# Optimization experiments

Measured on AMD Instinct MI355X. Metric: run time of the kernel, lower is better.

Reference implementation:

```python
import jax, jax.numpy as jnp
import numpy as np

HIDDEN, INPUT_DIM, OUTPUT_DIM, SEQ_LEN, BATCH = 1024, 1, 10, 784, 512


def make_discrete_hippo(N, L):
    # HiPPO-LegS matrix: A[n,k] = -sqrt(2n+1)sqrt(2k+1) for n>k, -(n+1) on diag; B[n]=sqrt(2n+1)
    q = np.arange(N, dtype=np.float64)
    P = np.sqrt(1.0 + 2.0 * q)
    A = -(np.tril(np.outer(P, P)) - np.diag(q))
    B = P[:, None]  # (N, 1)
    # bilinear (Tustin) discretization with step = 1/L
    step = 1.0 / L
    I = np.eye(N)
    M = np.linalg.inv(I - (step / 2.0) * A)
    Ad = M @ (I + (step / 2.0) * A)
    Bd = step * (M @ B)
    return jnp.asarray(Ad, jnp.float32), jnp.asarray(Bd, jnp.float32)


def setup_inputs() -> dict:
    key = jax.random.key(0)
    k1, k2, k3 = jax.random.split(key, 3)
    x = jax.random.normal(k1, (BATCH, SEQ_LEN, 1), jnp.float32)
    # C: xavier_uniform-like scale, shape (input_dim, hidden_dim)
    C = jax.random.normal(k2, (INPUT_DIM, HIDDEN), jnp.float32) / np.sqrt(HIDDEN).astype(np.float32)
    # final Dense(output_dim): kernel (input_dim, output_dim), bias (output_dim,)
    W = jax.random.normal(k3, (INPUT_DIM, OUTPUT_DIM), jnp.float32)
    b = jnp.zeros((OUTPUT_DIM,), jnp.float32)
    return {"x": x, "C": C, "W": W, "b": b}


def reference(x, C, W, b):
    Ad, Bd = make_discrete_hippo(HIDDEN, SEQ_LEN)  # constants (not learned)
    AdT = Ad.T                       # (N, N)
    Bvec = Bd[:, 0]                  # (N,)
    us = jnp.moveaxis(x[..., 0], 1, 0)  # (seq, batch) -- scan over time axis
    h0 = jnp.zeros((x.shape[0], HIDDEN), x.dtype)

    def step(h, u):
        # h_next = tanh(A h^T + B u)^T  ==  tanh(h @ A^T + u[:,None]*B)
        h_next = jnp.tanh(h @ AdT + u[:, None] * Bvec[None, :])  # (batch, N)
        y = h_next @ C.T                                         # (batch, input_dim)
        return h_next, y

    _, ys = jax.lax.scan(step, h0, us)  # ys: (seq, batch, input_dim)
    # Dense applied to all timesteps then [:, -1, :] == Dense on last timestep
    return ys[-1] @ W + b  # (batch, output_dim)
```

## Files before the change

### kernel.cpp

```cpp
#include <hip/hip_runtime.h>
#include <math.h>


#define SEQ     784
#define OUT_DIM 10
#define NW      4
#define CH      16
#define NCH     (SEQ/CH)
#define EPL     4

#if __has_builtin(__builtin_amdgcn_exp2f)
#define EXP2F(x) __builtin_amdgcn_exp2f(x)
#else
#define EXP2F(x) __expf(0.69314718055994531f * (x))
#endif

template<int CTRL, int ROW_MASK>
__device__ __forceinline__ float dpp_mov(float src, float old) {
    return __int_as_float(__builtin_amdgcn_update_dpp(
        __float_as_int(old), __float_as_int(src), CTRL, ROW_MASK, 0xf, false));
}
template<int CTRL>
__device__ __forceinline__ float dpp_bc0(float src) {
    return __int_as_float(__builtin_amdgcn_update_dpp(
        0, __float_as_int(src), CTRL, 0xf, 0xf, true));
}

__global__ __launch_bounds__(256, 2)
void ssm_hippo_scan(const float* __restrict__ x,
                    const float* __restrict__ C,
                    const float* __restrict__ W,
                    const float* __restrict__ bvec,
                    float* __restrict__ out)
{
    const int b    = blockIdx.x;
    const int tid  = threadIdx.x;
    const int wv   = tid >> 6;
    const int lane = tid & 63;

    __shared__ __align__(16) float u_s[SEQ];
    __shared__ __align__(16) float totB_s[NW-1][SEQ];
    __shared__ double part_s[NW];

    for (int t = tid; t < SEQ; t += 256) u_s[t] = x[b * SEQ + t];

    const double hdt  = 0.5 / (double)SEQ;
    const double L2E2 = 2.0 * 1.4426950408889634;

    float upc[EPL], ivd[EPL], ka[EPL], cB[EPL];
    float t10, t20, t21, t30, t31, t32;
    float Alev0, Alev1, Alev2, Alev3, Alev4, Alev5, Aexcl;
    float c2, n2c2;
    {
        double p[EPL], d[EPL], a[EPL], pdin[EPL], hp[EPL];
#pragma unroll
        for (int i = 0; i < EPL; ++i) {
            const int n = wv * 256 + lane * EPL + i;
            p[i]    = sqrt(1.0 + 2.0 * (double)n);
            d[i]    = 1.0 + hdt * (double)(n + 1);
            a[i]    = 1.0 - hdt * p[i] * p[i] / d[i];
            pdin[i] = p[i] / d[i];
            hp[i]   = 2.0 * hdt * p[i] / d[i];
            upc[i]  = (float)(L2E2 * hdt * p[i]);
            ivd[i]  = (float)(2.0 / d[i]);
        }
        const double ap0 = 1.0, ap1 = a[0], ap2 = a[0]*a[1], ap3 = a[0]*a[1]*a[2];
        ka[0] = (float)(-hp[0] * ap0);
        ka[1] = (float)(-hp[1] * ap1);
        ka[2] = (float)(-hp[2] * ap2);
        ka[3] = (float)(-hp[3] * ap3);
        cB[0] = (float)(a[1]*a[2]*a[3] * pdin[0]);
        cB[1] = (float)(a[2]*a[3] * pdin[1]);
        cB[2] = (float)(a[3] * pdin[2]);
        cB[3] = (float)(pdin[3]);
        t10 = (float)(-hp[1] * pdin[0]);
        t20 = (float)(-hp[2] * a[1] * pdin[0]);
        t21 = (float)(-hp[2] * pdin[1]);
        t30 = (float)(-hp[3] * a[2] * a[1] * pdin[0]);
        t31 = (float)(-hp[3] * a[2] * pdin[1]);
        t32 = (float)(-hp[3] * pdin[2]);

        float A = (float)(a[0]*a[1]*a[2]*a[3]);
        Alev0 = A; A *= dpp_mov<0x111, 0xf>(A, 1.0f);
        Alev1 = A; A *= dpp_mov<0x112, 0xf>(A, 1.0f);
        Alev2 = A; A *= dpp_mov<0x114, 0xf>(A, 1.0f);
        Alev3 = A; A *= dpp_mov<0x118, 0xf>(A, 1.0f);
        Alev4 = A; A *= dpp_mov<0x142, 0xa>(A, 1.0f);
        Alev5 = A; A *= dpp_mov<0x143, 0xc>(A, 1.0f);
        Aexcl = dpp_mov<0x138, 0xf>(A, 1.0f);

        c2   = (float)L2E2;
        n2c2 = (float)(-2.0 * L2E2);
    }

    float cF1 = 0.0f, cF2 = 0.0f, cF12 = 0.0f;
    {
        double n1 = 1.0, d1 = 1.0, n2 = 1.0, d2 = 1.0;
        for (int n = 256; n < 512; ++n) {
            n1 *= 1.0 - hdt * (double)n; d1 *= 1.0 + hdt * (double)(n + 1);
        }
        for (int n = 512; n < 768; ++n) {
            n2 *= 1.0 - hdt * (double)n; d2 *= 1.0 + hdt * (double)(n + 1);
        }
        const double Phi1 = n1 / d1, Phi2 = n2 / d2;
        cF1 = (float)Phi1; cF2 = (float)Phi2; cF12 = (float)(Phi1 * Phi2);
    }

    __syncthreads();

    float m0 = 0.0f, m1 = 0.0f, m2 = 0.0f, m3 = 0.0f;

#pragma unroll 1
    for (int tick = 0; tick < NCH + NW - 1; ++tick) {
        const int ch = tick - wv;
        if (0 <= ch && ch < NCH) {
            float4 u4[CH/4];
            float  Tin[CH];
            {
                const float4* up = (const float4*)&u_s[ch * CH];
#pragma unroll
                for (int q = 0; q < CH/4; ++q) u4[q] = up[q];
            }
            if (wv == 0) {
#pragma unroll
                for (int k = 0; k < CH; ++k) Tin[k] = 0.0f;
            } else if (wv == 1) {
                const float4* b0 = (const float4*)&totB_s[0][ch * CH];
#pragma unroll
                for (int q = 0; q < CH/4; ++q) {
                    const float4 v0 = b0[q];
                    Tin[4*q+0] = v0.x; Tin[4*q+1] = v0.y;
                    Tin[4*q+2] = v0.z; Tin[4*q+3] = v0.w;
                }
            } else if (wv == 2) {
                const float4* b0 = (const float4*)&totB_s[0][ch * CH];
                const float4* b1 = (const float4*)&totB_s[1][ch * CH];
#pragma unroll
                for (int q = 0; q < CH/4; ++q) {
                    const float4 v0 = b0[q], v1 = b1[q];
                    Tin[4*q+0] = fmaf(cF1, v0.x, v1.x);
                    Tin[4*q+1] = fmaf(cF1, v0.y, v1.y);
                    Tin[4*q+2] = fmaf(cF1, v0.z, v1.z);
                    Tin[4*q+3] = fmaf(cF1, v0.w, v1.w);
                }
            } else {
                const float4* b0 = (const float4*)&totB_s[0][ch * CH];
                const float4* b1 = (const float4*)&totB_s[1][ch * CH];
                const float4* b2 = (const float4*)&totB_s[2][ch * CH];
#pragma unroll
                for (int q = 0; q < CH/4; ++q) {
                    const float4 v0 = b0[q], v1 = b1[q], v2 = b2[q];
                    Tin[4*q+0] = fmaf(cF12, v0.x, fmaf(cF2, v1.x, v2.x));
                    Tin[4*q+1] = fmaf(cF12, v0.y, fmaf(cF2, v1.y, v2.y));
                    Tin[4*q+2] = fmaf(cF12, v0.z, fmaf(cF2, v1.z, v2.z));
                    Tin[4*q+3] = fmaf(cF12, v0.w, fmaf(cF2, v1.w, v2.w));
                }
            }
            float Bacc[CH];

#pragma unroll
            for (int k = 0; k < CH; ++k) {
                const float u = ((const float*)&u4[k>>2])[k&3];

                const float w0 = fmaf(upc[0], u, m0);
                const float w1 = fmaf(upc[1], u, m1);
                const float w2 = fmaf(upc[2], u, m2);
                const float w3 = fmaf(upc[3], u, m3);

                float B = fmaf(cB[0], w0,
                          fmaf(cB[1], w1,
                          fmaf(cB[2], w2, cB[3] * w3)));

                float Bin;
                Bin = dpp_bc0<0x111>(B);            B = fmaf(Alev0, Bin, B);
                Bin = dpp_bc0<0x112>(B);            B = fmaf(Alev1, Bin, B);
                Bin = dpp_bc0<0x114>(B);            B = fmaf(Alev2, Bin, B);
                Bin = dpp_bc0<0x118>(B);            B = fmaf(Alev3, Bin, B);
                Bin = dpp_mov<0x142, 0xa>(B, 0.0f); B = fmaf(Alev4, Bin, B);
                Bin = dpp_mov<0x143, 0xc>(B, 0.0f); B = fmaf(Alev5, Bin, B);
                Bacc[k] = B;

                const float Tst  = dpp_bc0<0x138>(B);
                const float Tent = fmaf(Aexcl, Tin[k], Tst);

                const float b0g = fmaf(ivd[0], w0, -m0);
                const float b1g = fmaf(ivd[1], w1, -m1);
                const float b2g = fmaf(ivd[2], w2, -m2);
                const float b3g = fmaf(ivd[3], w3, -m3);
                const float g0 = fmaf(ka[0], Tent, b0g);
                const float g1 = fmaf(ka[1], Tent, fmaf(t10, w0, b1g));
                const float g2 = fmaf(ka[2], Tent,
                                 fmaf(t20, w0, fmaf(t21, w1, b2g)));
                const float g3 = fmaf(ka[3], Tent,
                                 fmaf(t30, w0,
                                 fmaf(t31, w1, fmaf(t32, w2, b3g))));

                const float e0 = EXP2F(fminf(g0, 30.0f));
                const float e1 = EXP2F(fminf(g1, 30.0f));
                const float e2 = EXP2F(fminf(g2, 30.0f));
                const float e3 = EXP2F(fminf(g3, 30.0f));
                const float q0 = e0 + 1.0f, q1 = e1 + 1.0f;
                const float q2 = e2 + 1.0f, q3 = e3 + 1.0f;
                const float p01 = q0 * q1, p23 = q2 * q3;
                const float ip  = __builtin_amdgcn_rcpf(p01 * p23);
                const float i01 = p23 * ip;
                const float i23 = p01 * ip;
                m0 = fmaf(n2c2, q1 * i01, c2);
                m1 = fmaf(n2c2, q0 * i01, c2);
                m2 = fmaf(n2c2, q3 * i23, c2);
                m3 = fmaf(n2c2, q2 * i23, c2);
            }

            if (wv < NW - 1 && lane == 63) {
                float4* tp = (float4*)&totB_s[wv][ch * CH];
#pragma unroll
                for (int q = 0; q < CH/4; ++q)
                    tp[q] = make_float4(Bacc[4*q], Bacc[4*q+1],
                                        Bacc[4*q+2], Bacc[4*q+3]);
            }
        }
        __syncthreads();
    }

    double acc = 0.0;
    {
        const int base = wv * 256 + lane * EPL;
        acc = fma((double)C[base + 0], (double)m0, acc);
        acc = fma((double)C[base + 1], (double)m1, acc);
        acc = fma((double)C[base + 2], (double)m2, acc);
        acc = fma((double)C[base + 3], (double)m3, acc);
    }
#pragma unroll
    for (int off = 32; off > 0; off >>= 1)
        acc += __shfl_down(acc, off, 64);
    if (lane == 0) part_s[wv] = acc;
    __syncthreads();
    if (tid < OUT_DIM) {
        const double tot = (part_s[0] + part_s[1] + part_s[2] + part_s[3])
                         * 0.34657359027997264;
        out[b * OUT_DIM + tid] =
            (float)fma(tot, (double)W[tid], (double)bvec[tid]);
    }
}

extern "C" void kernel_launch(void* const* d_in, const int* in_sizes, int n_in,
                              void* d_out, int out_size, void* d_ws, size_t ws_size,
                              hipStream_t stream) {
    const float* x  = (const float*)d_in[0];
    const float* C  = (const float*)d_in[1];
    const float* W  = (const float*)d_in[2];
    const float* bv = (const float*)d_in[3];
    float* out      = (float*)d_out;
    hipLaunchKernelGGL(ssm_hippo_scan, dim3(512), dim3(256), 0, stream,
                       x, C, W, bv, out);
}
```

Measured before the change: 264.6 us.

## Split hidden state across 8 waves with 2 elements per lane

Doubles the block to 512 threads (8 waves) so each lane owns 2 hidden elements instead of 4, which shortens the per-step dependent arithmetic chain. The cross-wave carry changes from a direct sum over all earlier waves to a chained prefix: each wave folds its incoming carry into its outgoing total using a per-wave decay factor. This keeps the per-wave carry load to one buffer. The trade-off is a wavefront pipeline that is twice as deep (more ticks and barriers) and more waves per block, which affects occupancy.

Result: slower. 283.4 us (+7.1%).

```diff
diff --git a/kernel.cpp b/kernel.cpp
--- a/kernel.cpp
+++ b/kernel.cpp
@@ -4,10 +4,10 @@
 
 #define SEQ     784
 #define OUT_DIM 10
-#define NW      4
+#define NW      8
 #define CH      16
 #define NCH     (SEQ/CH)
-#define EPL     4
+#define EPL     2
 
 #if __has_builtin(__builtin_amdgcn_exp2f)
 #define EXP2F(x) __builtin_amdgcn_exp2f(x)
@@ -26,7 +26,7 @@
         0, __float_as_int(src), CTRL, 0xf, 0xf, true));
 }
 
-__global__ __launch_bounds__(256, 2)
+__global__ __launch_bounds__(512, 4)
 void ssm_hippo_scan(const float* __restrict__ x,
                     const float* __restrict__ C,
                     const float* __restrict__ W,
@@ -39,48 +39,40 @@
     const int lane = tid & 63;
 
     __shared__ __align__(16) float u_s[SEQ];
-    __shared__ __align__(16) float totB_s[NW-1][SEQ];
+    __shared__ __align__(16) float tot_s[NW-1][SEQ];
     __shared__ double part_s[NW];
 
-    for (int t = tid; t < SEQ; t += 256) u_s[t] = x[b * SEQ + t];
+    for (int t = tid; t < SEQ; t += 512) u_s[t] = x[b * SEQ + t];
 
     const double hdt  = 0.5 / (double)SEQ;
     const double L2E2 = 2.0 * 1.4426950408889634;
 
-    float upc[EPL], ivd[EPL], ka[EPL], cB[EPL];
-    float t10, t20, t21, t30, t31, t32;
+    float upc0, upc1, ivd0, ivd1, ka0, ka1, cB0, cB1, t10;
     float Alev0, Alev1, Alev2, Alev3, Alev4, Alev5, Aexcl;
-    float c2, n2c2;
+    float PhiW, c2, n2c2;
     {
-        double p[EPL], d[EPL], a[EPL], pdin[EPL], hp[EPL];
-#pragma unroll
-        for (int i = 0; i < EPL; ++i) {
-            const int n = wv * 256 + lane * EPL + i;
-            p[i]    = sqrt(1.0 + 2.0 * (double)n);
-            d[i]    = 1.0 + hdt * (double)(n + 1);
-            a[i]    = 1.0 - hdt * p[i] * p[i] / d[i];
-            pdin[i] = p[i] / d[i];
-            hp[i]   = 2.0 * hdt * p[i] / d[i];
-            upc[i]  = (float)(L2E2 * hdt * p[i]);
-            ivd[i]  = (float)(2.0 / d[i]);
-        }
-        const double ap0 = 1.0, ap1 = a[0], ap2 = a[0]*a[1], ap3 = a[0]*a[1]*a[2];
-        ka[0] = (float)(-hp[0] * ap0);
-        ka[1] = (float)(-hp[1] * ap1);
-        ka[2] = (float)(-hp[2] * ap2);
-        ka[3] = (float)(-hp[3] * ap3);
-        cB[0] = (float)(a[1]*a[2]*a[3] * pdin[0]);
-        cB[1] = (float)(a[2]*a[3] * pdin[1]);
-        cB[2] = (float)(a[3] * pdin[2]);
-        cB[3] = (float)(pdin[3]);
-        t10 = (float)(-hp[1] * pdin[0]);
-        t20 = (float)(-hp[2] * a[1] * pdin[0]);
-        t21 = (float)(-hp[2] * pdin[1]);
-        t30 = (float)(-hp[3] * a[2] * a[1] * pdin[0]);
-        t31 = (float)(-hp[3] * a[2] * pdin[1]);
-        t32 = (float)(-hp[3] * pdin[2]);
-
-        float A = (float)(a[0]*a[1]*a[2]*a[3]);
+        const int n0 = wv * 128 + lane * 2;
+        const int n1 = n0 + 1;
+        const double p0 = sqrt(1.0 + 2.0 * (double)n0);
+        const double p1 = sqrt(1.0 + 2.0 * (double)n1);
+        const double d0 = 1.0 + hdt * (double)(n0 + 1);
+        const double d1 = 1.0 + hdt * (double)(n1 + 1);
+        const double a0 = 1.0 - hdt * p0 * p0 / d0;
+        const double a1 = 1.0 - hdt * p1 * p1 / d1;
+        const double pdin0 = p0 / d0, pdin1 = p1 / d1;
+        const double hp0 = 2.0 * hdt * p0 / d0;
+        const double hp1 = 2.0 * hdt * p1 / d1;
+        upc0 = (float)(L2E2 * hdt * p0);
+        upc1 = (float)(L2E2 * hdt * p1);
+        ivd0 = (float)(2.0 / d0);
+        ivd1 = (float)(2.0 / d1);
+        ka0  = (float)(-hp0);
+        ka1  = (float)(-hp1 * a0);
+        cB0  = (float)(a1 * pdin0);
+        cB1  = (float)(pdin1);
+        t10  = (float)(-hp1 * pdin0);
+
+        float A = (float)(a0 * a1);
         Alev0 = A; A *= dpp_mov<0x111, 0xf>(A, 1.0f);
         Alev1 = A; A *= dpp_mov<0x112, 0xf>(A, 1.0f);
         Alev2 = A; A *= dpp_mov<0x114, 0xf>(A, 1.0f);
@@ -89,26 +81,20 @@
         Alev5 = A; A *= dpp_mov<0x143, 0xc>(A, 1.0f);
         Aexcl = dpp_mov<0x138, 0xf>(A, 1.0f);
 
+        double np = 1.0, dp = 1.0;
+        for (int n = wv * 128; n < wv * 128 + 128; ++n) {
+            np *= 1.0 - hdt * (double)n;
+            dp *= 1.0 + hdt * (double)(n + 1);
+        }
+        PhiW = (float)(np / dp);
+
         c2   = (float)L2E2;
         n2c2 = (float)(-2.0 * L2E2);
     }
 
-    float cF1 = 0.0f, cF2 = 0.0f, cF12 = 0.0f;
-    {
-        double n1 = 1.0, d1 = 1.0, n2 = 1.0, d2 = 1.0;
-        for (int n = 256; n < 512; ++n) {
-            n1 *= 1.0 - hdt * (double)n; d1 *= 1.0 + hdt * (double)(n + 1);
-        }
-        for (int n = 512; n < 768; ++n) {
-            n2 *= 1.0 - hdt * (double)n; d2 *= 1.0 + hdt * (double)(n + 1);
-        }
-        const double Phi1 = n1 / d1, Phi2 = n2 / d2;
-        cF1 = (float)Phi1; cF2 = (float)Phi2; cF12 = (float)(Phi1 * Phi2);
-    }
-
     __syncthreads();
 
-    float m0 = 0.0f, m1 = 0.0f, m2 = 0.0f, m3 = 0.0f;
+    float m0 = 0.0f, m1 = 0.0f;
 
 #pragma unroll 1
     for (int tick = 0; tick < NCH + NW - 1; ++tick) {
@@ -124,37 +110,14 @@
             if (wv == 0) {
 #pragma unroll
                 for (int k = 0; k < CH; ++k) Tin[k] = 0.0f;
-            } else if (wv == 1) {
-                const float4* b0 = (const float4*)&totB_s[0][ch * CH];
+            } else {
+                const float4* b0 = (const float4*)&tot_s[wv - 1][ch * CH];
 #pragma unroll
                 for (int q = 0; q < CH/4; ++q) {
                     const float4 v0 = b0[q];
                     Tin[4*q+0] = v0.x; Tin[4*q+1] = v0.y;
                     Tin[4*q+2] = v0.z; Tin[4*q+3] = v0.w;
                 }
-            } else if (wv == 2) {
-                const float4* b0 = (const float4*)&totB_s[0][ch * CH];
-                const float4* b1 = (const float4*)&totB_s[1][ch * CH];
-#pragma unroll
-                for (int q = 0; q < CH/4; ++q) {
-                    const float4 v0 = b0[q], v1 = b1[q];
-                    Tin[4*q+0] = fmaf(cF1, v0.x, v1.x);
-                    Tin[4*q+1] = fmaf(cF1, v0.y, v1.y);
-                    Tin[4*q+2] = fmaf(cF1, v0.z, v1.z);
-                    Tin[4*q+3] = fmaf(cF1, v0.w, v1.w);
-                }
-            } else {
-                const float4* b0 = (const float4*)&totB_s[0][ch * CH];
-                const float4* b1 = (const float4*)&totB_s[1][ch * CH];
-                const float4* b2 = (const float4*)&totB_s[2][ch * CH];
-#pragma unroll
-                for (int q = 0; q < CH/4; ++q) {
-                    const float4 v0 = b0[q], v1 = b1[q], v2 = b2[q];
-                    Tin[4*q+0] = fmaf(cF12, v0.x, fmaf(cF2, v1.x, v2.x));
-                    Tin[4*q+1] = fmaf(cF12, v0.y, fmaf(cF2, v1.y, v2.y));
-                    Tin[4*q+2] = fmaf(cF12, v0.z, fmaf(cF2, v1.z, v2.z));
-                    Tin[4*q+3] = fmaf(cF12, v0.w, fmaf(cF2, v1.w, v2.w));
-                }
             }
             float Bacc[CH];
 
@@ -162,14 +125,10 @@
             for (int k = 0; k < CH; ++k) {
                 const float u = ((const float*)&u4[k>>2])[k&3];
 
-                const float w0 = fmaf(upc[0], u, m0);
-                const float w1 = fmaf(upc[1], u, m1);
-                const float w2 = fmaf(upc[2], u, m2);
-                const float w3 = fmaf(upc[3], u, m3);
-
-                float B = fmaf(cB[0], w0,
-                          fmaf(cB[1], w1,
-                          fmaf(cB[2], w2, cB[3] * w3)));
+                const float w0 = fmaf(upc0, u, m0);
+                const float w1 = fmaf(upc1, u, m1);
+
+                float B = fmaf(cB0, w0, cB1 * w1);
 
                 float Bin;
                 Bin = dpp_bc0<0x111>(B);            B = fmaf(Alev0, Bin, B);
@@ -183,40 +142,27 @@
                 const float Tst  = dpp_bc0<0x138>(B);
                 const float Tent = fmaf(Aexcl, Tin[k], Tst);
 
-                const float b0g = fmaf(ivd[0], w0, -m0);
-                const float b1g = fmaf(ivd[1], w1, -m1);
-                const float b2g = fmaf(ivd[2], w2, -m2);
-                const float b3g = fmaf(ivd[3], w3, -m3);
-                const float g0 = fmaf(ka[0], Tent, b0g);
-                const float g1 = fmaf(ka[1], Tent, fmaf(t10, w0, b1g));
-                const float g2 = fmaf(ka[2], Tent,
-                                 fmaf(t20, w0, fmaf(t21, w1, b2g)));
-                const float g3 = fmaf(ka[3], Tent,
-                                 fmaf(t30, w0,
-                                 fmaf(t31, w1, fmaf(t32, w2, b3g))));
+                const float g0 = fmaf(ka0, Tent, fmaf(ivd0, w0, -m0));
+                const float g1 = fmaf(ka1, Tent,
+                                 fmaf(t10, w0, fmaf(ivd1, w1, -m1)));
 
                 const float e0 = EXP2F(fminf(g0, 30.0f));
                 const float e1 = EXP2F(fminf(g1, 30.0f));
-                const float e2 = EXP2F(fminf(g2, 30.0f));
-                const float e3 = EXP2F(fminf(g3, 30.0f));
                 const float q0 = e0 + 1.0f, q1 = e1 + 1.0f;
-                const float q2 = e2 + 1.0f, q3 = e3 + 1.0f;
-                const float p01 = q0 * q1, p23 = q2 * q3;
-                const float ip  = __builtin_amdgcn_rcpf(p01 * p23);
-                const float i01 = p23 * ip;
-                const float i23 = p01 * ip;
-                m0 = fmaf(n2c2, q1 * i01, c2);
-                m1 = fmaf(n2c2, q0 * i01, c2);
-                m2 = fmaf(n2c2, q3 * i23, c2);
-                m3 = fmaf(n2c2, q2 * i23, c2);
+                const float ip = __builtin_amdgcn_rcpf(q0 * q1);
+                m0 = fmaf(n2c2, q1 * ip, c2);
+                m1 = fmaf(n2c2, q0 * ip, c2);
             }
 
             if (wv < NW - 1 && lane == 63) {
-                float4* tp = (float4*)&totB_s[wv][ch * CH];
+                float4* tp = (float4*)&tot_s[wv][ch * CH];
 #pragma unroll
                 for (int q = 0; q < CH/4; ++q)
-                    tp[q] = make_float4(Bacc[4*q], Bacc[4*q+1],
-                                        Bacc[4*q+2], Bacc[4*q+3]);
+                    tp[q] = make_float4(
+                        fmaf(PhiW, Tin[4*q+0], Bacc[4*q+0]),
+                        fmaf(PhiW, Tin[4*q+1], Bacc[4*q+1]),
+                        fmaf(PhiW, Tin[4*q+2], Bacc[4*q+2]),
+                        fmaf(PhiW, Tin[4*q+3], Bacc[4*q+3]));
             }
         }
         __syncthreads();
@@ -224,11 +170,9 @@
 
     double acc = 0.0;
     {
-        const int base = wv * 256 + lane * EPL;
+        const int base = wv * 128 + lane * 2;
         acc = fma((double)C[base + 0], (double)m0, acc);
         acc = fma((double)C[base + 1], (double)m1, acc);
-        acc = fma((double)C[base + 2], (double)m2, acc);
-        acc = fma((double)C[base + 3], (double)m3, acc);
     }
 #pragma unroll
     for (int off = 32; off > 0; off >>= 1)
@@ -236,8 +180,10 @@
     if (lane == 0) part_s[wv] = acc;
     __syncthreads();
     if (tid < OUT_DIM) {
-        const double tot = (part_s[0] + part_s[1] + part_s[2] + part_s[3])
-                         * 0.34657359027997264;
+        double tot = 0.0;
+#pragma unroll
+        for (int wq = 0; wq < NW; ++wq) tot += part_s[wq];
+        tot *= 0.34657359027997264;
         out[b * OUT_DIM + tid] =
             (float)fma(tot, (double)W[tid], (double)bvec[tid]);
     }
@@ -251,6 +197,6 @@
     const float* W  = (const float*)d_in[2];
     const float* bv = (const float*)d_in[3];
     float* out      = (float*)d_out;
-    hipLaunchKernelGGL(ssm_hippo_scan, dim3(512), dim3(256), 0, stream,
+    hipLaunchKernelGGL(ssm_hippo_scan, dim3(512), dim3(512), 0, stream,
                        x, C, W, bv, out);
 }
```
